# Kernel optimization log

Measured on AMD Instinct MI355X. Metric: run time of the kernel, lower is better.

Reference implementation:

```python
import jax, jax.numpy as jnp
import numpy as np

H = 16          # num_attention_heads
D = 1024        # hidden_size
HD = D // H     # attention_head_size = 64


def setup_inputs() -> dict:
    key = jax.random.key(0)
    ks = jax.random.split(key, 9)
    s = 1.0 / np.sqrt(D)
    return {
        "hidden_states": jax.random.normal(ks[0], (4, 1024, D), jnp.float32),
        "encoder_hidden_states": jax.random.normal(ks[1], (4, 1024, D), jnp.float32),
        "attention_mask": jnp.zeros((4, 1, 1, 2048), jnp.float32),
        "Wq": jax.random.normal(ks[2], (D, D), jnp.float32) * s,
        "bq": jnp.zeros((D,), jnp.float32),
        "Wk": jax.random.normal(ks[3], (D, D), jnp.float32) * s,
        "bk": jnp.zeros((D,), jnp.float32),
        "Wv": jax.random.normal(ks[4], (D, D), jnp.float32) * s,
        "bv": jnp.zeros((D,), jnp.float32),
    }


def _split_heads(x):
    # [B, S, D] -> [B, H, S, HD]
    B, S, _ = x.shape
    return x.reshape(B, S, H, HD).transpose(0, 2, 1, 3)


def reference(hidden_states, encoder_hidden_states, attention_mask, Wq, bq, Wk, bk, Wv, bv):
    # KV over concat(encoder, decoder); Q over decoder hidden states only.
    all_hidden = jnp.concatenate([encoder_hidden_states, hidden_states], axis=1)  # [B, Skv, D]
    q = _split_heads(hidden_states @ Wq + bq)        # [B, H, Sq, HD]
    k = _split_heads(all_hidden @ Wk + bk)           # [B, H, Skv, HD]
    v = _split_heads(all_hidden @ Wv + bv)           # [B, H, Skv, HD]

    scores = jnp.einsum("bhqd,bhkd->bhqk", q, k) / np.sqrt(HD).astype(np.float32)
    scores = scores + attention_mask                 # additive mask, broadcast
    probs = jax.nn.softmax(scores, axis=-1)          # dropout p=0 (eval)
    ctx = jnp.einsum("bhqk,bhkd->bhqd", probs, v)    # [B, H, Sq, HD]
    B, _, Sq, _ = ctx.shape
    return ctx.transpose(0, 2, 1, 3).reshape(B, Sq, D)
```

## Files before the change

kernel.cpp:

```cpp
#include <hip/hip_runtime.h>


typedef _Float16 f16;
typedef __attribute__((ext_vector_type(4))) _Float16 half4;
typedef __attribute__((ext_vector_type(8))) _Float16 half8;
typedef __attribute__((ext_vector_type(4))) float floatx4;
typedef __attribute__((ext_vector_type(16))) float floatx16;
typedef __attribute__((ext_vector_type(4))) unsigned int uint4v;

#define GLOAD16(gp, lp)                                                        \
    __builtin_amdgcn_global_load_lds(                                          \
        (const __attribute__((address_space(1))) void*)(gp),                   \
        (__attribute__((address_space(3))) void*)(lp), 16, 0, 0)

__global__ void wt_kernel(const float* __restrict__ Wq, const float* __restrict__ Wk,
                          const float* __restrict__ Wv, f16* __restrict__ Wtq,
                          f16* __restrict__ Wtk, f16* __restrict__ Wtv) {
    __shared__ float tile[32][33];
    const float* W = (blockIdx.z == 0) ? Wq : (blockIdx.z == 1) ? Wk : Wv;
    f16* Wt = (blockIdx.z == 0) ? Wtq : (blockIdx.z == 1) ? Wtk : Wtv;
    int k0 = blockIdx.y * 32, n0 = blockIdx.x * 32;
    int tx = threadIdx.x, ty = threadIdx.y;
    #pragma unroll
    for (int i = 0; i < 32; i += 8)
        tile[ty + i][tx] = W[(k0 + ty + i) * 1024 + n0 + tx];
    __syncthreads();
    #pragma unroll
    for (int i = 0; i < 32; i += 8)
        Wt[(n0 + ty + i) * 1024 + k0 + tx] = (f16)tile[tx][ty + i];
}

__global__ void cvt_kernel(const float* __restrict__ hid, const float* __restrict__ enc,
                           f16* __restrict__ Aall) {
    int t = blockIdx.x * 256 + threadIdx.x;
    int rowg = t >> 7, col = (t & 127) * 8;
    int b = rowg >> 11, r = rowg & 2047;
    const float* src = (r < 1024 ? enc + ((size_t)b * 1024 + r) * 1024
                                 : hid + ((size_t)b * 1024 + (r - 1024)) * 1024) + col;
    float4 v0 = *(const float4*)src, v1 = *(const float4*)(src + 4);
    half8 o;
    o[0] = (f16)v0.x; o[1] = (f16)v0.y; o[2] = (f16)v0.z; o[3] = (f16)v0.w;
    o[4] = (f16)v1.x; o[5] = (f16)v1.y; o[6] = (f16)v1.z; o[7] = (f16)v1.w;
    *(half8*)(Aall + (size_t)rowg * 1024 + col) = o;
}

__global__ void maskscale_kernel(const float* __restrict__ mask, float* __restrict__ maskS) {
    const float LOG2E = 1.4426950408889634f;
    int i = blockIdx.x * 256 + threadIdx.x;
    float4 v = ((const float4*)mask)[i];
    v.x *= LOG2E; v.y *= LOG2E; v.z *= LOG2E; v.w *= LOG2E;
    ((float4*)maskS)[i] = v;
}

__launch_bounds__(256)
__global__ void qkv_gemm(const f16* __restrict__ Aall, const f16* __restrict__ Wt,
                         const float* __restrict__ bias, f16* __restrict__ out, int mode) {
    __shared__ f16 As[128 * 32];
    __shared__ f16 Bs[128 * 32];

    int tid = threadIdx.x;
    int m0 = blockIdx.x * 128, n0 = blockIdx.y * 128;
    int wid = tid >> 6, lane = tid & 63;
    int wm = (wid >> 1) * 64, wn = (wid & 1) * 64;
    int lr = lane & 15, lg = lane >> 4;

    floatx4 acc[4][4];
    #pragma unroll
    for (int i = 0; i < 4; i++)
        #pragma unroll
        for (int j = 0; j < 4; j++) acc[i][j] = (floatx4)(0.f);

    int trow = tid >> 2, tcol = (tid & 3) * 8;
    const f16 *a0g, *a1g;
    {
        int mA0 = m0 + trow, mA1 = mA0 + 64;
        if (mode == 0) {
            int b0 = mA0 >> 10, b1 = mA1 >> 10;
            a0g = Aall + ((size_t)(b0 * 2048 + 1024 + (mA0 & 1023))) * 1024 + tcol;
            a1g = Aall + ((size_t)(b1 * 2048 + 1024 + (mA1 & 1023))) * 1024 + tcol;
        } else {
            a0g = Aall + (size_t)mA0 * 1024 + tcol;
            a1g = Aall + (size_t)mA1 * 1024 + tcol;
        }
    }
    const f16* b0g = Wt + (size_t)(n0 + trow) * 1024 + tcol;
    const f16* b1g = Wt + (size_t)(n0 + trow + 64) * 1024 + tcol;
    f16* lA0 = &As[tid * 8];
    f16* lA1 = &As[tid * 8 + 2048];
    f16* lB0 = &Bs[tid * 8];
    f16* lB1 = &Bs[tid * 8 + 2048];

    for (int k0 = 0; k0 < 1024; k0 += 32) {
        GLOAD16(a0g + k0, lA0);
        GLOAD16(a1g + k0, lA1);
        GLOAD16(b0g + k0, lB0);
        GLOAD16(b1g + k0, lB1);
        __syncthreads();

        half8 a[4], bf[4];
        #pragma unroll
        for (int i = 0; i < 4; i++)
            a[i] = *(const half8*)&As[(wm + i * 16 + lr) * 32 + lg * 8];
        #pragma unroll
        for (int j = 0; j < 4; j++)
            bf[j] = *(const half8*)&Bs[(wn + j * 16 + lr) * 32 + lg * 8];
        __builtin_amdgcn_s_setprio(1);
        #pragma unroll
        for (int i = 0; i < 4; i++)
            #pragma unroll
            for (int j = 0; j < 4; j++)
                acc[i][j] = __builtin_amdgcn_mfma_f32_16x16x32_f16(a[i], bf[j], acc[i][j], 0, 0, 0);
        __builtin_amdgcn_s_setprio(0);
        __syncthreads();
    }

    if (mode == 2) {
        #pragma unroll
        for (int i = 0; i < 4; i++) {
            int mbase = m0 + wm + i * 16 + lg * 4;
            int b = mbase >> 11, s = mbase & 2047;
            #pragma unroll
            for (int j = 0; j < 4; j++) {
                int n = n0 + wn + j * 16 + lr;
                int h = n >> 6, d = n & 63;
                float bv = bias[n];
                half4 w;
                #pragma unroll
                for (int r = 0; r < 4; r++) w[r] = (f16)(acc[i][j][r] + bv);
                *(half4*)(out + ((size_t)((b * 16 + h) * 64 + d)) * 2048 + s) = w;
            }
        }
    } else {
        int Sout = (mode == 0) ? 1024 : 2048;
        #pragma unroll
        for (int i = 0; i < 4; i++) {
            int mbase = m0 + wm + i * 16 + lg * 4;
            #pragma unroll
            for (int j = 0; j < 4; j++) {
                int n = n0 + wn + j * 16 + lr;
                int h = n >> 6, d = n & 63;
                float bv = bias[n];
                #pragma unroll
                for (int r = 0; r < 4; r++) {
                    int m = mbase + r;
                    int b = (mode == 0) ? (m >> 10) : (m >> 11);
                    int s = (mode == 0) ? (m & 1023) : (m & 2047);
                    out[((size_t)(b * 16 + h) * Sout + s) * 64 + d] = (f16)(acc[i][j][r] + bv);
                }
            }
        }
    }
}

__device__ inline half8 pack_swap(float s0, float s1, float s2, float s3,
                                  float s4, float s5, float s6, float s7) {
    unsigned a0 = __builtin_bit_cast(unsigned, __builtin_amdgcn_cvt_pkrtz(s0, s1));
    unsigned b0 = __builtin_bit_cast(unsigned, __builtin_amdgcn_cvt_pkrtz(s4, s5));
    unsigned a1 = __builtin_bit_cast(unsigned, __builtin_amdgcn_cvt_pkrtz(s2, s3));
    unsigned b1 = __builtin_bit_cast(unsigned, __builtin_amdgcn_cvt_pkrtz(s6, s7));
    asm("v_permlane32_swap_b32 %0, %1" : "+v"(a0), "+v"(b0));
    asm("v_permlane32_swap_b32 %0, %1" : "+v"(a1), "+v"(b1));
    uint4v w = {a0, a1, b0, b1};
    return __builtin_bit_cast(half8, w);
}

__device__ inline half8 pack_noswap(float s0, float s1, float s2, float s3,
                                    float s4, float s5, float s6, float s7) {
    unsigned w0 = __builtin_bit_cast(unsigned, __builtin_amdgcn_cvt_pkrtz(s0, s1));
    unsigned w1 = __builtin_bit_cast(unsigned, __builtin_amdgcn_cvt_pkrtz(s2, s3));
    unsigned w2 = __builtin_bit_cast(unsigned, __builtin_amdgcn_cvt_pkrtz(s4, s5));
    unsigned w3 = __builtin_bit_cast(unsigned, __builtin_amdgcn_cvt_pkrtz(s6, s7));
    uint4v w = {w0, w1, w2, w3};
    return __builtin_bit_cast(half8, w);
}

struct F4x4 { float4 a, b, c, d; };

__launch_bounds__(256)
__global__ void attn_kernel(const f16* __restrict__ Q, const f16* __restrict__ K,
                            const f16* __restrict__ Vt, const float* __restrict__ maskS,
                            float* __restrict__ out) {
    __shared__ f16 Kt[64 * 72];
    __shared__ f16 Vtt[64 * 72];

    int tid = threadIdx.x;
    int wid = tid >> 6, lane = tid & 63;
    int l31 = lane & 31, l5 = lane >> 5;

    int bid = blockIdx.x + 8 * blockIdx.y;
    int xcd = bid & 7, w = bid >> 3;
    int bh = xcd * 8 + (w >> 3);
    int xblk = w & 7;
    int b = bh >> 4;
    int q = xblk * 128 + wid * 32 + l31;

    half8 pa, pcode;
    #pragma unroll
    for (int j = 0; j < 8; j++) { pa[j] = (f16)0; pcode[j] = (f16)(8 * l5 + j); }
    if (l31 < 16 && (l31 >> 3) == l5) pa[l31 & 7] = (f16)1;
    floatx16 pd = __builtin_amdgcn_mfma_f32_32x32x16_f16(pa, pcode, (floatx16)0.f, 0, 0, 0);
    float r4 = __shfl(pd[0], 32);
    bool twoblk = (r4 > 6.0f);

    const f16* qrow = Q + ((size_t)bh * 1024 + q) * 64;
    half8 qf[4];
    if (!twoblk) {
        #pragma unroll
        for (int ks = 0; ks < 4; ks++)
            qf[ks] = *(const half8*)(qrow + ks * 16 + l5 * 8);
    } else {
        #pragma unroll
        for (int ks = 0; ks < 4; ks++) {
            half4 lo = *(const half4*)(qrow + ks * 16 + 4 * l5);
            half4 hi = *(const half4*)(qrow + ks * 16 + 8 + 4 * l5);
            qf[ks][0] = lo[0]; qf[ks][1] = lo[1]; qf[ks][2] = lo[2]; qf[ks][3] = lo[3];
            qf[ks][4] = hi[0]; qf[ks][5] = hi[1]; qf[ks][6] = hi[2]; qf[ks][7] = hi[3];
        }
    }
    const f16 qs = (f16)(0.125f * 1.4426950408889634f);
    #pragma unroll
    for (int ks = 0; ks < 4; ks++)
        #pragma unroll
        for (int x = 0; x < 8; x++) qf[ks][x] *= qs;

    floatx16 o0 = (floatx16)0.f, o1 = (floatx16)0.f;
    float m_run = 8.0f, l_run = 0.f;

    int sr = tid >> 2, sc = (tid & 3) * 16;
    const f16* Ksrc = K + ((size_t)bh * 2048 + sr) * 64 + sc;
    const f16* Vsrc = Vt + ((size_t)(bh * 64 + sr)) * 2048 + sc;
    const float* Mb = maskS + b * 2048 + 4 * l5;

    half8 rk0 = *(const half8*)(Ksrc);
    half8 rk1 = *(const half8*)(Ksrc + 8);
    half8 rv0 = *(const half8*)(Vsrc);
    half8 rv1 = *(const half8*)(Vsrc + 8);

    for (int kv0 = 0; kv0 < 2048; kv0 += 64) {
        __syncthreads();
        *(half8*)&Kt[sr * 72 + sc]      = rk0;
        *(half8*)&Kt[sr * 72 + sc + 8]  = rk1;
        *(half8*)&Vtt[sr * 72 + sc]     = rv0;
        *(half8*)&Vtt[sr * 72 + sc + 8] = rv1;
        __syncthreads();
        if (kv0 < 2048 - 64) {
            rk0 = *(const half8*)(Ksrc + (size_t)(kv0 + 64) * 64);
            rk1 = *(const half8*)(Ksrc + (size_t)(kv0 + 64) * 64 + 8);
            rv0 = *(const half8*)(Vsrc + kv0 + 64);
            rv1 = *(const half8*)(Vsrc + kv0 + 64 + 8);
        }

        F4x4 t0, t1;
        t0.a = *(const float4*)(Mb + kv0);      t0.b = *(const float4*)(Mb + kv0 + 8);
        t0.c = *(const float4*)(Mb + kv0 + 16); t0.d = *(const float4*)(Mb + kv0 + 24);
        t1.a = *(const float4*)(Mb + kv0 + 32); t1.b = *(const float4*)(Mb + kv0 + 40);
        t1.c = *(const float4*)(Mb + kv0 + 48); t1.d = *(const float4*)(Mb + kv0 + 56);
        floatx16 sf0 = __builtin_bit_cast(floatx16, t0);
        floatx16 sf1 = __builtin_bit_cast(floatx16, t1);

        __builtin_amdgcn_s_setprio(1);
        #pragma unroll
        for (int ks = 0; ks < 4; ks++) {
            half8 k0 = *(const half8*)&Kt[l31 * 72 + ks * 16 + l5 * 8];
            half8 k1 = *(const half8*)&Kt[(32 + l31) * 72 + ks * 16 + l5 * 8];
            sf0 = __builtin_amdgcn_mfma_f32_32x32x16_f16(k0, qf[ks], sf0, 0, 0, 0);
            sf1 = __builtin_amdgcn_mfma_f32_32x32x16_f16(k1, qf[ks], sf1, 0, 0, 0);
        }
        __builtin_amdgcn_s_setprio(0);

        float pmax = -1e30f;
        #pragma unroll
        for (int r = 0; r < 16; r++)
            pmax = fmaxf(pmax, fmaxf(sf0[r], sf1[r]));

        if (!__all(pmax - m_run <= 8.0f)) {
            float rmax = fmaxf(pmax, __shfl_xor(pmax, 32));
            float mnew = fmaxf(m_run, rmax);
            float alpha = exp2f(m_run - mnew);
            l_run *= alpha;
            #pragma unroll
            for (int r = 0; r < 16; r++) { o0[r] *= alpha; o1[r] *= alpha; }
            m_run = mnew;
        }

        float ls = 0.f;
        #pragma unroll
        for (int r = 0; r < 16; r++) {
            float p0 = exp2f(sf0[r] - m_run);
            float p1 = exp2f(sf1[r] - m_run);
            sf0[r] = p0; sf1[r] = p1;
            ls += p0 + p1;
        }
        ls += __shfl_xor(ls, 32);
        l_run += ls;

        half8 pb[4];
        if (!twoblk) {
            pb[0] = pack_swap(sf0[0], sf0[1], sf0[2], sf0[3], sf0[4], sf0[5], sf0[6], sf0[7]);
            pb[1] = pack_swap(sf0[8], sf0[9], sf0[10], sf0[11], sf0[12], sf0[13], sf0[14], sf0[15]);
            pb[2] = pack_swap(sf1[0], sf1[1], sf1[2], sf1[3], sf1[4], sf1[5], sf1[6], sf1[7]);
            pb[3] = pack_swap(sf1[8], sf1[9], sf1[10], sf1[11], sf1[12], sf1[13], sf1[14], sf1[15]);
        } else {
            pb[0] = pack_noswap(sf0[0], sf0[1], sf0[2], sf0[3], sf0[4], sf0[5], sf0[6], sf0[7]);
            pb[1] = pack_noswap(sf0[8], sf0[9], sf0[10], sf0[11], sf0[12], sf0[13], sf0[14], sf0[15]);
            pb[2] = pack_noswap(sf1[0], sf1[1], sf1[2], sf1[3], sf1[4], sf1[5], sf1[6], sf1[7]);
            pb[3] = pack_noswap(sf1[8], sf1[9], sf1[10], sf1[11], sf1[12], sf1[13], sf1[14], sf1[15]);
        }

        __builtin_amdgcn_s_setprio(1);
        #pragma unroll
        for (int kb = 0; kb < 4; kb++) {
            half8 v0 = *(const half8*)&Vtt[l31 * 72 + kb * 16 + l5 * 8];
            half8 v1 = *(const half8*)&Vtt[(32 + l31) * 72 + kb * 16 + l5 * 8];
            o0 = __builtin_amdgcn_mfma_f32_32x32x16_f16(v0, pb[kb], o0, 0, 0, 0);
            o1 = __builtin_amdgcn_mfma_f32_32x32x16_f16(v1, pb[kb], o1, 0, 0, 0);
        }
        __builtin_amdgcn_s_setprio(0);
    }

    int h = bh & 15;
    float inv = 1.f / l_run;
    float* orow = out + ((size_t)(b * 1024 + q)) * 1024 + h * 64;
    #pragma unroll
    for (int g = 0; g < 4; g++) {
        float4 r0 = {o0[4 * g] * inv, o0[4 * g + 1] * inv, o0[4 * g + 2] * inv, o0[4 * g + 3] * inv};
        float4 r1 = {o1[4 * g] * inv, o1[4 * g + 1] * inv, o1[4 * g + 2] * inv, o1[4 * g + 3] * inv};
        *(float4*)&orow[8 * g + 4 * l5]      = r0;
        *(float4*)&orow[32 + 8 * g + 4 * l5] = r1;
    }
}

extern "C" void kernel_launch(void* const* d_in, const int* in_sizes, int n_in,
                              void* d_out, int out_size, void* d_ws, size_t ws_size,
                              hipStream_t stream) {
    const float* hid  = (const float*)d_in[0];
    const float* enc  = (const float*)d_in[1];
    const float* mask = (const float*)d_in[2];
    const float* Wq   = (const float*)d_in[3];
    const float* bq   = (const float*)d_in[4];
    const float* Wk   = (const float*)d_in[5];
    const float* bk   = (const float*)d_in[6];
    const float* Wv   = (const float*)d_in[7];
    const float* bv   = (const float*)d_in[8];
    float* out = (float*)d_out;

    char* ws = (char*)d_ws;
    f16* Wtq  = (f16*)(ws + ((size_t)0 << 20));
    f16* Wtk  = (f16*)(ws + ((size_t)2 << 20));
    f16* Wtv  = (f16*)(ws + ((size_t)4 << 20));
    f16* Aall = (f16*)(ws + ((size_t)6 << 20));
    f16* Qw   = (f16*)(ws + ((size_t)22 << 20));
    f16* Kw   = (f16*)(ws + ((size_t)30 << 20));
    f16* Vtw  = (f16*)(ws + ((size_t)46 << 20));
    float* maskS = (float*)(ws + ((size_t)62 << 20));

    wt_kernel<<<dim3(32, 32, 3), dim3(32, 8), 0, stream>>>(Wq, Wk, Wv, Wtq, Wtk, Wtv);
    cvt_kernel<<<4096, 256, 0, stream>>>(hid, enc, Aall);
    maskscale_kernel<<<8, 256, 0, stream>>>(mask, maskS);

    qkv_gemm<<<dim3(32, 8), 256, 0, stream>>>(Aall, Wtq, bq, Qw, 0);
    qkv_gemm<<<dim3(64, 8), 256, 0, stream>>>(Aall, Wtk, bk, Kw, 1);
    qkv_gemm<<<dim3(64, 8), 256, 0, stream>>>(Aall, Wtv, bv, Vtw, 2);

    attn_kernel<<<dim3(8, 64), 256, 0, stream>>>(Qw, Kw, Vtw, maskS, out);
}
```

Measured before the change: 174.4 us.

## Double-buffer GEMM and attention LDS, merge QKV launches, fold mask scaling

The QKV GEMM now double-buffers its LDS tiles so the next K-slice is fetched while the current one is multiplied, which removes one barrier per iteration. The three projection GEMMs are merged into a single launch over a z dimension, with early exit for the smaller Q grid. The attention kernel double-buffers its K/V LDS tiles and keeps the log2e-scaled mask in LDS, which removes the separate maskscale kernel. The cost is twice the LDS footprint, which may reduce occupancy, plus some idle blocks in the merged grid.

After: 155.1 us. -11.1%, faster.

```diff
diff --git a/kernel.cpp b/kernel.cpp
--- a/kernel.cpp
+++ b/kernel.cpp
@@ -44,19 +44,21 @@
     *(half8*)(Aall + (size_t)rowg * 1024 + col) = o;
 }
 
-__global__ void maskscale_kernel(const float* __restrict__ mask, float* __restrict__ maskS) {
-    const float LOG2E = 1.4426950408889634f;
-    int i = blockIdx.x * 256 + threadIdx.x;
-    float4 v = ((const float4*)mask)[i];
-    v.x *= LOG2E; v.y *= LOG2E; v.z *= LOG2E; v.w *= LOG2E;
-    ((float4*)maskS)[i] = v;
-}
-
 __launch_bounds__(256)
-__global__ void qkv_gemm(const f16* __restrict__ Aall, const f16* __restrict__ Wt,
-                         const float* __restrict__ bias, f16* __restrict__ out, int mode) {
-    __shared__ f16 As[128 * 32];
-    __shared__ f16 Bs[128 * 32];
+__global__ void qkv_gemm(const f16* __restrict__ Aall,
+                         const f16* __restrict__ Wtq, const f16* __restrict__ Wtk,
+                         const f16* __restrict__ Wtv,
+                         const float* __restrict__ bq, const float* __restrict__ bk,
+                         const float* __restrict__ bv,
+                         f16* __restrict__ Qw, f16* __restrict__ Kw, f16* __restrict__ Vtw) {
+    int mode = blockIdx.z;
+    if (mode == 0 && blockIdx.x >= 32) return;
+    __shared__ f16 As[2][128 * 32];
+    __shared__ f16 Bs[2][128 * 32];
+
+    const f16* Wt = (mode == 0) ? Wtq : (mode == 1) ? Wtk : Wtv;
+    const float* bias = (mode == 0) ? bq : (mode == 1) ? bk : bv;
+    f16* out = (mode == 0) ? Qw : (mode == 1) ? Kw : Vtw;
 
     int tid = threadIdx.x;
     int m0 = blockIdx.x * 128, n0 = blockIdx.y * 128;
@@ -85,25 +87,29 @@
     }
     const f16* b0g = Wt + (size_t)(n0 + trow) * 1024 + tcol;
     const f16* b1g = Wt + (size_t)(n0 + trow + 64) * 1024 + tcol;
-    f16* lA0 = &As[tid * 8];
-    f16* lA1 = &As[tid * 8 + 2048];
-    f16* lB0 = &Bs[tid * 8];
-    f16* lB1 = &Bs[tid * 8 + 2048];
-
+
+    GLOAD16(a0g, &As[0][tid * 8]);
+    GLOAD16(a1g, &As[0][tid * 8 + 2048]);
+    GLOAD16(b0g, &Bs[0][tid * 8]);
+    GLOAD16(b1g, &Bs[0][tid * 8 + 2048]);
+    __syncthreads();
+
+    int cur = 0;
     for (int k0 = 0; k0 < 1024; k0 += 32) {
-        GLOAD16(a0g + k0, lA0);
-        GLOAD16(a1g + k0, lA1);
-        GLOAD16(b0g + k0, lB0);
-        GLOAD16(b1g + k0, lB1);
-        __syncthreads();
-
+        if (k0 < 992) {
+            int nx = cur ^ 1;
+            GLOAD16(a0g + k0 + 32, &As[nx][tid * 8]);
+            GLOAD16(a1g + k0 + 32, &As[nx][tid * 8 + 2048]);
+            GLOAD16(b0g + k0 + 32, &Bs[nx][tid * 8]);
+            GLOAD16(b1g + k0 + 32, &Bs[nx][tid * 8 + 2048]);
+        }
         half8 a[4], bf[4];
         #pragma unroll
         for (int i = 0; i < 4; i++)
-            a[i] = *(const half8*)&As[(wm + i * 16 + lr) * 32 + lg * 8];
+            a[i] = *(const half8*)&As[cur][(wm + i * 16 + lr) * 32 + lg * 8];
         #pragma unroll
         for (int j = 0; j < 4; j++)
-            bf[j] = *(const half8*)&Bs[(wn + j * 16 + lr) * 32 + lg * 8];
+            bf[j] = *(const half8*)&Bs[cur][(wn + j * 16 + lr) * 32 + lg * 8];
         __builtin_amdgcn_s_setprio(1);
         #pragma unroll
         for (int i = 0; i < 4; i++)
@@ -112,6 +118,7 @@
                 acc[i][j] = __builtin_amdgcn_mfma_f32_16x16x32_f16(a[i], bf[j], acc[i][j], 0, 0, 0);
         __builtin_amdgcn_s_setprio(0);
         __syncthreads();
+        cur ^= 1;
     }
 
     if (mode == 2) {
@@ -174,15 +181,15 @@
     return __builtin_bit_cast(half8, w);
 }
 
-struct F4x4 { float4 a, b, c, d; };
-
 __launch_bounds__(256)
 __global__ void attn_kernel(const f16* __restrict__ Q, const f16* __restrict__ K,
-                            const f16* __restrict__ Vt, const float* __restrict__ maskS,
+                            const f16* __restrict__ Vt, const float* __restrict__ mask,
                             float* __restrict__ out) {
-    __shared__ f16 Kt[64 * 72];
-    __shared__ f16 Vtt[64 * 72];
-
+    __shared__ f16 Kt[2][64 * 72];
+    __shared__ f16 Vtt[2][64 * 72];
+    __shared__ float maskLds[2048];
+
+    const float LOG2E = 1.4426950408889634f;
     int tid = threadIdx.x;
     int wid = tid >> 6, lane = tid & 63;
     int l31 = lane & 31, l5 = lane >> 5;
@@ -202,6 +209,13 @@
     float r4 = __shfl(pd[0], 32);
     bool twoblk = (r4 > 6.0f);
 
+    const float* maskp = mask + b * 2048;
+    for (int i = tid; i < 512; i += 256) {
+        float4 mv = ((const float4*)maskp)[i];
+        mv.x *= LOG2E; mv.y *= LOG2E; mv.z *= LOG2E; mv.w *= LOG2E;
+        ((float4*)maskLds)[i] = mv;
+    }
+
     const f16* qrow = Q + ((size_t)bh * 1024 + q) * 64;
     half8 qf[4];
     if (!twoblk) {
@@ -229,40 +243,54 @@
     int sr = tid >> 2, sc = (tid & 3) * 16;
     const f16* Ksrc = K + ((size_t)bh * 2048 + sr) * 64 + sc;
     const f16* Vsrc = Vt + ((size_t)(bh * 64 + sr)) * 2048 + sc;
-    const float* Mb = maskS + b * 2048 + 4 * l5;
 
     half8 rk0 = *(const half8*)(Ksrc);
     half8 rk1 = *(const half8*)(Ksrc + 8);
     half8 rv0 = *(const half8*)(Vsrc);
     half8 rv1 = *(const half8*)(Vsrc + 8);
-
+    *(half8*)&Kt[0][sr * 72 + sc]      = rk0;
+    *(half8*)&Kt[0][sr * 72 + sc + 8]  = rk1;
+    *(half8*)&Vtt[0][sr * 72 + sc]     = rv0;
+    *(half8*)&Vtt[0][sr * 72 + sc + 8] = rv1;
+    rk0 = *(const half8*)(Ksrc + (size_t)64 * 64);
+    rk1 = *(const half8*)(Ksrc + (size_t)64 * 64 + 8);
+    rv0 = *(const half8*)(Vsrc + 64);
+    rv1 = *(const half8*)(Vsrc + 64 + 8);
+    __syncthreads();
+
+    int cur = 0;
     for (int kv0 = 0; kv0 < 2048; kv0 += 64) {
-        __syncthreads();
-        *(half8*)&Kt[sr * 72 + sc]      = rk0;
-        *(half8*)&Kt[sr * 72 + sc + 8]  = rk1;
-        *(half8*)&Vtt[sr * 72 + sc]     = rv0;
-        *(half8*)&Vtt[sr * 72 + sc + 8] = rv1;
-        __syncthreads();
         if (kv0 < 2048 - 64) {
-            rk0 = *(const half8*)(Ksrc + (size_t)(kv0 + 64) * 64);
-            rk1 = *(const half8*)(Ksrc + (size_t)(kv0 + 64) * 64 + 8);
-            rv0 = *(const half8*)(Vsrc + kv0 + 64);
-            rv1 = *(const half8*)(Vsrc + kv0 + 64 + 8);
-        }
-
-        F4x4 t0, t1;
-        t0.a = *(const float4*)(Mb + kv0);      t0.b = *(const float4*)(Mb + kv0 + 8);
-        t0.c = *(const float4*)(Mb + kv0 + 16); t0.d = *(const float4*)(Mb + kv0 + 24);
-        t1.a = *(const float4*)(Mb + kv0 + 32); t1.b = *(const float4*)(Mb + kv0 + 40);
-        t1.c = *(const float4*)(Mb + kv0 + 48); t1.d = *(const float4*)(Mb + kv0 + 56);
-        floatx16 sf0 = __builtin_bit_cast(floatx16, t0);
-        floatx16 sf1 = __builtin_bit_cast(floatx16, t1);
+            int nx = cur ^ 1;
+            *(half8*)&Kt[nx][sr * 72 + sc]      = rk0;
+            *(half8*)&Kt[nx][sr * 72 + sc + 8]  = rk1;
+            *(half8*)&Vtt[nx][sr * 72 + sc]     = rv0;
+            *(half8*)&Vtt[nx][sr * 72 + sc + 8] = rv1;
+            if (kv0 < 2048 - 128) {
+                rk0 = *(const half8*)(Ksrc + (size_t)(kv0 + 128) * 64);
+                rk1 = *(const half8*)(Ksrc + (size_t)(kv0 + 128) * 64 + 8);
+                rv0 = *(const half8*)(Vsrc + kv0 + 128);
+                rv1 = *(const half8*)(Vsrc + kv0 + 128 + 8);
+            }
+        }
+
+        floatx16 sf0, sf1;
+        #pragma unroll
+        for (int g = 0; g < 4; g++) {
+            float4 mk0 = *(const float4*)&maskLds[kv0 + 8 * g + 4 * l5];
+            float4 mk1 = *(const float4*)&maskLds[kv0 + 32 + 8 * g + 4 * l5];
+            #pragma unroll
+            for (int i = 0; i < 4; i++) {
+                sf0[4 * g + i] = ((const float*)&mk0)[i];
+                sf1[4 * g + i] = ((const float*)&mk1)[i];
+            }
+        }
 
         __builtin_amdgcn_s_setprio(1);
         #pragma unroll
         for (int ks = 0; ks < 4; ks++) {
-            half8 k0 = *(const half8*)&Kt[l31 * 72 + ks * 16 + l5 * 8];
-            half8 k1 = *(const half8*)&Kt[(32 + l31) * 72 + ks * 16 + l5 * 8];
+            half8 k0 = *(const half8*)&Kt[cur][l31 * 72 + ks * 16 + l5 * 8];
+            half8 k1 = *(const half8*)&Kt[cur][(32 + l31) * 72 + ks * 16 + l5 * 8];
             sf0 = __builtin_amdgcn_mfma_f32_32x32x16_f16(k0, qf[ks], sf0, 0, 0, 0);
             sf1 = __builtin_amdgcn_mfma_f32_32x32x16_f16(k1, qf[ks], sf1, 0, 0, 0);
         }
@@ -310,12 +338,15 @@
         __builtin_amdgcn_s_setprio(1);
         #pragma unroll
         for (int kb = 0; kb < 4; kb++) {
-            half8 v0 = *(const half8*)&Vtt[l31 * 72 + kb * 16 + l5 * 8];
-            half8 v1 = *(const half8*)&Vtt[(32 + l31) * 72 + kb * 16 + l5 * 8];
+            half8 v0 = *(const half8*)&Vtt[cur][l31 * 72 + kb * 16 + l5 * 8];
+            half8 v1 = *(const half8*)&Vtt[cur][(32 + l31) * 72 + kb * 16 + l5 * 8];
             o0 = __builtin_amdgcn_mfma_f32_32x32x16_f16(v0, pb[kb], o0, 0, 0, 0);
             o1 = __builtin_amdgcn_mfma_f32_32x32x16_f16(v1, pb[kb], o1, 0, 0, 0);
         }
         __builtin_amdgcn_s_setprio(0);
+
+        __syncthreads();
+        cur ^= 1;
     }
 
     int h = bh & 15;
@@ -352,15 +383,11 @@
     f16* Qw   = (f16*)(ws + ((size_t)22 << 20));
     f16* Kw   = (f16*)(ws + ((size_t)30 << 20));
     f16* Vtw  = (f16*)(ws + ((size_t)46 << 20));
-    float* maskS = (float*)(ws + ((size_t)62 << 20));
 
     wt_kernel<<<dim3(32, 32, 3), dim3(32, 8), 0, stream>>>(Wq, Wk, Wv, Wtq, Wtk, Wtv);
     cvt_kernel<<<4096, 256, 0, stream>>>(hid, enc, Aall);
-    maskscale_kernel<<<8, 256, 0, stream>>>(mask, maskS);
-
-    qkv_gemm<<<dim3(32, 8), 256, 0, stream>>>(Aall, Wtq, bq, Qw, 0);
-    qkv_gemm<<<dim3(64, 8), 256, 0, stream>>>(Aall, Wtk, bk, Kw, 1);
-    qkv_gemm<<<dim3(64, 8), 256, 0, stream>>>(Aall, Wtv, bv, Vtw, 2);
-
-    attn_kernel<<<dim3(8, 64), 256, 0, stream>>>(Qw, Kw, Vtw, maskS, out);
-}
+
+    qkv_gemm<<<dim3(64, 8, 3), 256, 0, stream>>>(Aall, Wtq, Wtk, Wtv, bq, bk, bv, Qw, Kw, Vtw);
+
+    attn_kernel<<<dim3(8, 64), 256, 0, stream>>>(Qw, Kw, Vtw, mask, out);
+}
```
